# Kernel tuning notes

Measured on AMD Instinct MI355X. Metric: run time of the kernel, lower is better.

The kernel has to match this reference:

```python
import jax, jax.numpy as jnp
import numpy as np

B, S, D, M, HID, THETA = 8, 4096, 128, 256, 256, 4096


def _impulse_response():
    """Build discretized LTI (A,B) via ZOH and the impulse response H [M, S]."""
    Q = jnp.arange(M, dtype=jnp.float32).reshape(-1, 1)          # [M,1]
    R = (2.0 * Q + 1.0) / THETA                                   # [M,1]
    ii, jj = jnp.meshgrid(jnp.arange(M), jnp.arange(M), indexing='ij')
    # (-1)^(i-j+1): -1 when (i-j) even, +1 when odd
    sign = jnp.where((ii - jj) % 2 == 0, -1.0, 1.0)
    A = R * jnp.where(ii < jj, -1.0, sign)                        # [M,M]
    Bv = R * jnp.where(jnp.arange(M).reshape(-1, 1) % 2 == 0, 1.0, -1.0)  # [M,1]
    # zero-order-hold discretization via matrix exponential of augmented system
    aug = jnp.zeros((M + 1, M + 1), dtype=jnp.float32)
    aug = aug.at[:M, :M].set(A).at[:M, M].set(Bv[:, 0])
    expA = jax.scipy.linalg.expm(aug)
    Ad, Bd = expA[:M, :M], expA[:M, M:M + 1]
    # H[:, i] = Ad^i @ Bd
    def step(Ai, _):
        return Ad @ Ai, (Ai @ Bd)[:, 0]
    _, Hs = jax.lax.scan(step, jnp.eye(M, dtype=jnp.float32), None, length=S)
    return Hs.T  # [M, S]


def setup_inputs() -> dict:
    key = jax.random.key(0)
    k1, k2, k3 = jax.random.split(key, 3)
    x = jax.random.normal(k1, (B, S, D), dtype=jnp.float32)
    W_u = jax.random.normal(k2, (D, 1), dtype=jnp.float32) / np.sqrt(D)
    b_u = jnp.zeros((1,), dtype=jnp.float32)
    W_h = jax.random.normal(k3, (M + D, HID), dtype=jnp.float32) / np.sqrt(M + D)
    b_h = jnp.zeros((HID,), dtype=jnp.float32)
    H = _impulse_response()  # [M, S], fixed (non-trainable) impulse response
    return {"x": x, "W_u": W_u, "b_u": b_u, "W_h": W_h, "b_h": b_h, "H": H}


def reference(x, W_u, b_u, W_h, b_h, H):
    batch, seq_len, _ = x.shape
    n = 2 * seq_len
    # u_t = relu(W_u x_t)  -> [B, S, 1]
    u = jax.nn.relu(jnp.einsum('bsd,do->bso', x, W_u) + b_u)
    fft_H = jnp.fft.rfft(H, n=n, axis=-1)                 # [M, S+1]
    fft_u = jnp.fft.rfft(u[..., 0], n=n, axis=-1)         # [B, S+1]
    temp = fft_u[:, None, :] * fft_H[None, :, :]          # [B, M, S+1] complex
    m = jnp.fft.irfft(temp, n=n, axis=-1)[:, :, :seq_len]  # [B, M, S]
    m = jnp.transpose(m, (0, 2, 1))                       # [B, S, M]
    input_h = jnp.concatenate([m, x], axis=-1)            # [B, S, M+D]
    h = jax.nn.relu(jnp.einsum('bsf,fh->bsh', input_h, W_h) + b_h)
    h_n = h[:, -1, :]
    return (h, h_n)
```

## Files before the change

kernel.cpp:

```cpp
#include <hip/hip_runtime.h>

#define S_LEN 4096
#define B_SZ 8
#define HN_OFF 8388608
#define CPROWS 544

typedef __attribute__((ext_vector_type(8))) short short8;
typedef __attribute__((ext_vector_type(4))) float f32x4;

typedef const __attribute__((address_space(1))) unsigned int as1_u32;
typedef __attribute__((address_space(3))) unsigned int as3_u32;

__device__ __forceinline__ void gload16(const short* g, short* l) {
  __builtin_amdgcn_global_load_lds((as1_u32*)g, (as3_u32*)l, 16, 0, 0);
}

__device__ __forceinline__ short f2bf(float f) {
  union { float f; unsigned u; } v; v.f = f;
  unsigned r = v.u + 0x7FFFu + ((v.u >> 16) & 1u);
  return (short)(r >> 16);
}

__global__ __launch_bounds__(256) void k_prep(const float* __restrict__ x,
                                              const float* __restrict__ Wu,
                                              const float* __restrict__ bu,
                                              const float* __restrict__ H,
                                              const float* __restrict__ Wh,
                                              short* __restrict__ cp,
                                              short* __restrict__ xb,
                                              short* __restrict__ Ht,
                                              short* __restrict__ wht) {
  int bx = blockIdx.x;
  if (bx >= 8520) {
    int j = (bx - 8520) * 256 + threadIdx.x;
    if (j < 256 * 384) {
      int n = j / 384, k = j % 384;
      wht[j] = f2bf(Wh[k * 256 + n]);
    }
    return;
  }
  if (bx >= 8264) {
    __shared__ short tile[64][72];
    int bx2 = bx - 8264;
    int t0 = (bx2 >> 2) << 6, q0 = (bx2 & 3) << 6;
    int tid = threadIdx.x;
    int r = tid >> 2, c0 = (tid & 3) << 4;
    const float* src = H + (size_t)(q0 + r) * S_LEN + t0 + c0;
    #pragma unroll
    for (int v4 = 0; v4 < 4; ++v4) {
      float4 hv = *(const float4*)(src + 4 * v4);
      tile[r][c0 + 4 * v4]     = f2bf(hv.x);
      tile[r][c0 + 4 * v4 + 1] = f2bf(hv.y);
      tile[r][c0 + 4 * v4 + 2] = f2bf(hv.z);
      tile[r][c0 + 4 * v4 + 3] = f2bf(hv.w);
    }
    __syncthreads();
    int s2 = tid >> 2, qc = (tid & 3) << 4;
    short8 o0, o1;
    #pragma unroll
    for (int j2 = 0; j2 < 8; ++j2) {
      o0[j2] = tile[qc + j2][s2];
      o1[j2] = tile[qc + 8 + j2][s2];
    }
    short* dst = Ht + (size_t)(t0 + s2) * 256 + q0 + qc;
    *(short8*)dst       = o0;
    *(short8*)(dst + 8) = o1;
    return;
  }
  if (bx >= 8192) {
    int idx = (bx - 8192) * 256 + threadIdx.x;
    if (idx < 18432) {
      int j = idx & 7;
      int r = 508 + ((idx >> 3) % 36);
      int rem = (idx >> 3) / 36;
      int p = rem & 7;
      int b = rem >> 3;
      int e = 8 * r + p + j;
      if (e >= S_LEN)
        cp[((size_t)(b * 8 + p) * CPROWS + r) * 8 + j] = 0;
    }
    return;
  }
  int row = bx * 4 + (threadIdx.x >> 6);
  int l = threadIdx.x & 63;
  float2 xv = *(const float2*)(x + (size_t)row * 128 + 2 * l);
  float2 wv = *(const float2*)(Wu + 2 * l);
  float s = xv.x * wv.x + xv.y * wv.y;
  #pragma unroll
  for (int m = 32; m >= 1; m >>= 1) s += __shfl_xor(s, m, 64);
  unsigned pack = (((unsigned)f2bf(xv.y) & 0xFFFFu) << 16) | ((unsigned)f2bf(xv.x) & 0xFFFFu);
  *(unsigned*)(xb + (size_t)row * 128 + 2 * l) = pack;
  float v = s + bu[0];
  v = v > 0.0f ? v : 0.0f;
  short vb = f2bf(v);
  if (l < 8) {
    int t = row & (S_LEN - 1);
    int b = row >> 12;
    int e = (S_LEN - 1) - t;
    int p = l;
    if (e >= p) {
      int d = e - p;
      cp[((size_t)(b * 8 + p) * CPROWS + (d >> 3)) * 8 + (d & 7)] = vb;
    }
  }
}

__global__ __launch_bounds__(256) void k_g(const short* __restrict__ wht,
                                           const short* __restrict__ Ht,
                                           short* __restrict__ Gt) {
  int nt = blockIdx.x & 1, tt = blockIdx.x >> 1;
  int n0 = nt << 7, t0 = tt << 7;
  int tid = threadIdx.x;
  int lane = tid & 63, wid = tid >> 6;
  int wr = wid >> 1, wc = wid & 1;
  int lm = lane & 15, kg = lane >> 4;

  const short* Abase = wht + (size_t)(n0 + wr * 64 + lm) * 384 + 8 * kg;
  const short* Bbase = Ht  + (size_t)(t0 + wc * 64 + lm) * 256 + 8 * kg;

  f32x4 acc[4][4];
  #pragma unroll
  for (int ii = 0; ii < 4; ++ii)
    #pragma unroll
    for (int jn = 0; jn < 4; ++jn)
      acc[ii][jn] = (f32x4){0.0f, 0.0f, 0.0f, 0.0f};

  #pragma unroll
  for (int c = 0; c < 4; ++c) {
    short8 a[8], bf[8];
    #pragma unroll
    for (int mf = 0; mf < 4; ++mf)
      #pragma unroll
      for (int ks = 0; ks < 2; ++ks)
        a[mf * 2 + ks] = *(const short8*)(Abase + mf * 16 * 384 + c * 64 + ks * 32);
    #pragma unroll
    for (int nf = 0; nf < 4; ++nf)
      #pragma unroll
      for (int ks = 0; ks < 2; ++ks)
        bf[nf * 2 + ks] = *(const short8*)(Bbase + nf * 16 * 256 + c * 64 + ks * 32);
    #pragma unroll
    for (int ks = 0; ks < 2; ++ks)
      #pragma unroll
      for (int mf = 0; mf < 4; ++mf)
        #pragma unroll
        for (int nf = 0; nf < 4; ++nf)
          acc[mf][nf] = __builtin_amdgcn_mfma_f32_16x16x32_bf16(a[mf * 2 + ks], bf[nf * 2 + ks], acc[mf][nf], 0, 0, 0);
  }

  #pragma unroll
  for (int mf = 0; mf < 4; ++mf)
    #pragma unroll
    for (int nf = 0; nf < 4; ++nf)
      #pragma unroll
      for (int j = 0; j < 4; ++j) {
        int n = n0 + wr * 64 + mf * 16 + kg * 4 + j;
        int t = t0 + wc * 64 + nf * 16 + lm;
        Gt[(size_t)n * S_LEN + t] = f2bf(acc[mf][nf][j]);
      }
}

__global__ __launch_bounds__(256, 2) void k_fused(const short* __restrict__ cp,
                                                  const short* __restrict__ Gt,
                                                  const short* __restrict__ xb,
                                                  const short* __restrict__ wht,
                                                  const float* __restrict__ bh,
                                                  float* __restrict__ out) {
  __shared__ __attribute__((aligned(16))) short Bt[2][128 * 128];
  __shared__ __attribute__((aligned(16))) short Aw[2][2048];

  int i = blockIdx.x;
  int j  = i >> 1, lo = i & 1;
  int jj = j & 127;
  int fj = (j >> 7) ? (31 - (jj >> 3)) : (jj >> 3);
  int st = lo ? (31 - fj) : fj;
  int nt = lo;
  int b  = j & 7;
  int s0 = st << 7, n0 = nt << 7;

  int tid = threadIdx.x;
  int lane = tid & 63, wid = tid >> 6;
  int wr = wid >> 1, wc = wid & 1;
  int lm = lane & 15, kg = lane >> 4;
  int l3 = lane >> 3, l7 = lane & 7;
  int lm7 = lm & 7;

  const short* bS0 = Gt + (size_t)(n0 + wid * 32 + kg) * S_LEN + ((lm ^ kg) << 3);
  const short* bS1 = Gt + (size_t)(n0 + wid * 32 + kg) * S_LEN + ((lm ^ kg ^ 4) << 3);

  int asbase = 496 - 16 * st;
  const short* aSrc = cp + ((size_t)(b * 8 + (l7 ^ l3)) * CPROWS + asbase + wid * 8 + l3) * 8;

  const short* xS0 = xb + (size_t)(b * S_LEN + s0 + wid * 32 + kg) * 128 + ((lm ^ kg) << 3);
  const short* xS1 = xb + (size_t)(b * S_LEN + s0 + wid * 32 + kg) * 128 + ((lm ^ kg ^ 4) << 3);

  int dbase = 127 - 64 * wr - lm + 8 * kg;
  int aof[10];
  #pragma unroll
  for (int v = 0; v < 10; ++v) {
    int d = dbase + 16 * v - 48;
    aof[v] = ((d & ~7) | ((d & 7) ^ ((d >> 3) & 7))) << 3;
  }

  int bof[16];
  #pragma unroll
  for (int nf = 0; nf < 4; ++nf)
    #pragma unroll
    for (int ks = 0; ks < 4; ++ks)
      bof[nf * 4 + ks] = (wc * 64 + nf * 16 + lm) * 128 + (((4 * ks + kg) ^ lm7) << 3);

  int aofx[16];
  #pragma unroll
  for (int mf = 0; mf < 4; ++mf)
    #pragma unroll
    for (int ks = 0; ks < 4; ++ks)
      aofx[mf * 4 + ks] = (wr * 64 + mf * 16 + lm) * 128 + (((4 * ks + kg) ^ lm7) << 3);

  f32x4 acc[4][4];
  #pragma unroll
  for (int ii = 0; ii < 4; ++ii)
    #pragma unroll
    for (int jn = 0; jn < 4; ++jn)
      acc[ii][jn] = (f32x4){0.0f, 0.0f, 0.0f, 0.0f};

  int nchunks = st + 1;

  auto STAGE = [&](int cc) {
    int slot = cc & 1;
    int coff = cc * 128;
    #pragma unroll
    for (int e = 0; e < 4; ++e) {
      gload16(bS0 + (size_t)(8 * e) * S_LEN + coff,     &Bt[slot][(wid * 32 + 8 * e) * 128]);
      gload16(bS1 + (size_t)(8 * e + 4) * S_LEN + coff, &Bt[slot][(wid * 32 + 8 * e + 4) * 128]);
    }
    gload16(aSrc + coff, &Aw[slot][wid * 512]);
  };
  auto STAGE_X = [&]() {
    int slot = (st + 1) & 1;
    #pragma unroll
    for (int e = 0; e < 4; ++e) {
      gload16(xS0 + (size_t)(8 * e) * 128,     &Bt[slot][(wid * 32 + 8 * e) * 128]);
      gload16(xS1 + (size_t)(8 * e + 4) * 128, &Bt[slot][(wid * 32 + 8 * e + 4) * 128]);
    }
  };

  STAGE(0);

  for (int c = 0; c < nchunks; ++c) {
    asm volatile("s_waitcnt vmcnt(0) lgkmcnt(0)\n\ts_barrier" ::: "memory");
    if (c + 1 < nchunks) STAGE(c + 1);
    else STAGE_X();
    const short* AwB = &Aw[c & 1][0];
    const short* BtB = &Bt[c & 1][0];
    short8 A10[10];
    #pragma unroll
    for (int v = 0; v < 10; ++v) A10[v] = *(const short8*)(AwB + aof[v]);
    short8 Bf[16];
    #pragma unroll
    for (int ii = 0; ii < 16; ++ii) Bf[ii] = *(const short8*)(BtB + bof[ii]);
    __builtin_amdgcn_s_setprio(1);
    #pragma unroll
    for (int ks = 0; ks < 4; ++ks)
      #pragma unroll
      for (int mf = 0; mf < 4; ++mf)
        #pragma unroll
        for (int nf = 0; nf < 4; ++nf)
          acc[mf][nf] = __builtin_amdgcn_mfma_f32_16x16x32_bf16(
              A10[2 * ks - mf + 3], Bf[nf * 4 + ks], acc[mf][nf], 0, 0, 0);
    __builtin_amdgcn_s_setprio(0);
  }

  short8 Bx[16];
  #pragma unroll
  for (int nf = 0; nf < 4; ++nf)
    #pragma unroll
    for (int ks = 0; ks < 4; ++ks)
      Bx[nf * 4 + ks] = *(const short8*)(wht + (size_t)(n0 + wc * 64 + nf * 16 + lm) * 384 + 256 + 32 * ks + 8 * kg);
  asm volatile("s_waitcnt vmcnt(0) lgkmcnt(0)\n\ts_barrier" ::: "memory");
  {
    const short* XtB = &Bt[(st + 1) & 1][0];
    short8 Ax[16];
    #pragma unroll
    for (int ii = 0; ii < 16; ++ii) Ax[ii] = *(const short8*)(XtB + aofx[ii]);
    __builtin_amdgcn_s_setprio(1);
    #pragma unroll
    for (int ks = 0; ks < 4; ++ks)
      #pragma unroll
      for (int mf = 0; mf < 4; ++mf)
        #pragma unroll
        for (int nf = 0; nf < 4; ++nf)
          acc[mf][nf] = __builtin_amdgcn_mfma_f32_16x16x32_bf16(
              Ax[mf * 4 + ks], Bx[nf * 4 + ks], acc[mf][nf], 0, 0, 0);
    __builtin_amdgcn_s_setprio(0);
  }

  #pragma unroll
  for (int mf = 0; mf < 4; ++mf)
    #pragma unroll
    for (int nf = 0; nf < 4; ++nf) {
      int n = n0 + wc * 64 + nf * 16 + lm;
      float bias = bh[n];
      #pragma unroll
      for (int j2 = 0; j2 < 4; ++j2) {
        int s = s0 + wr * 64 + mf * 16 + kg * 4 + j2;
        float v = acc[mf][nf][j2] + bias;
        v = v > 0.0f ? v : 0.0f;
        out[(size_t)(b * S_LEN + s) * 256 + n] = v;
        if (s == S_LEN - 1)
          out[HN_OFF + b * 256 + n] = v;
      }
    }
}

extern "C" void kernel_launch(void* const* d_in, const int* in_sizes, int n_in,
                              void* d_out, int out_size, void* d_ws, size_t ws_size,
                              hipStream_t stream) {
  const float* x  = (const float*)d_in[0];
  const float* Wu = (const float*)d_in[1];
  const float* bu = (const float*)d_in[2];
  const float* Wh = (const float*)d_in[3];
  const float* bh = (const float*)d_in[4];
  const float* H  = (const float*)d_in[5];
  float* out = (float*)d_out;

  char* ws = (char*)d_ws;
  short* cp  = (short*)(ws);
  short* wht = (short*)(ws + 557056);
  short* xb  = (short*)(ws + 753664);
  short* Ht  = (short*)(ws + 9142272);
  short* Gt  = (short*)(ws + 11239424);

  k_prep<<<8904, 256, 0, stream>>>(x, Wu, bu, H, Wh, cp, xb, Ht, wht);
  k_g   <<<64,   256, 0, stream>>>(wht, Ht, Gt);
  k_fused<<<512, 256, 0, stream>>>(cp, Gt, xb, wht, bh, out);
}
```

Measured before the change: 77.72 us.

## Restructure fused GEMM into 4-slot 64-wide K pipeline with split-phase staging

Changes the fused Toeplitz+x GEMM main loop from a 2-slot buffer of 128-wide K chunks to a 4-slot ring of 64-wide chunks, prefetching two chunks ahead. Waits use partial vmcnt counts instead of draining everything. Each chunk is split into two half-phases that interleave LDS fragment reads, the next stage's global-to-LDS loads and MFMA bursts, separated by barriers. The x·W_h tail is folded into the same loop and its weights are loaded per chunk rather than up front. This aims to overlap memory latency with MFMA work and cut register pressure, at the cost of more barriers and more complex vmcnt bookkeeping.

```diff
diff --git a/kernel.cpp b/kernel.cpp
--- a/kernel.cpp
+++ b/kernel.cpp
@@ -20,6 +20,24 @@
   unsigned r = v.u + 0x7FFFu + ((v.u >> 16) & 1u);
   return (short)(r >> 16);
 }
+
+#define MFMA16(Aa, Bb) \
+  acc[0][0] = __builtin_amdgcn_mfma_f32_16x16x32_bf16(Aa##0, Bb##0, acc[0][0], 0, 0, 0); \
+  acc[0][1] = __builtin_amdgcn_mfma_f32_16x16x32_bf16(Aa##0, Bb##1, acc[0][1], 0, 0, 0); \
+  acc[0][2] = __builtin_amdgcn_mfma_f32_16x16x32_bf16(Aa##0, Bb##2, acc[0][2], 0, 0, 0); \
+  acc[0][3] = __builtin_amdgcn_mfma_f32_16x16x32_bf16(Aa##0, Bb##3, acc[0][3], 0, 0, 0); \
+  acc[1][0] = __builtin_amdgcn_mfma_f32_16x16x32_bf16(Aa##1, Bb##0, acc[1][0], 0, 0, 0); \
+  acc[1][1] = __builtin_amdgcn_mfma_f32_16x16x32_bf16(Aa##1, Bb##1, acc[1][1], 0, 0, 0); \
+  acc[1][2] = __builtin_amdgcn_mfma_f32_16x16x32_bf16(Aa##1, Bb##2, acc[1][2], 0, 0, 0); \
+  acc[1][3] = __builtin_amdgcn_mfma_f32_16x16x32_bf16(Aa##1, Bb##3, acc[1][3], 0, 0, 0); \
+  acc[2][0] = __builtin_amdgcn_mfma_f32_16x16x32_bf16(Aa##2, Bb##0, acc[2][0], 0, 0, 0); \
+  acc[2][1] = __builtin_amdgcn_mfma_f32_16x16x32_bf16(Aa##2, Bb##1, acc[2][1], 0, 0, 0); \
+  acc[2][2] = __builtin_amdgcn_mfma_f32_16x16x32_bf16(Aa##2, Bb##2, acc[2][2], 0, 0, 0); \
+  acc[2][3] = __builtin_amdgcn_mfma_f32_16x16x32_bf16(Aa##2, Bb##3, acc[2][3], 0, 0, 0); \
+  acc[3][0] = __builtin_amdgcn_mfma_f32_16x16x32_bf16(Aa##3, Bb##0, acc[3][0], 0, 0, 0); \
+  acc[3][1] = __builtin_amdgcn_mfma_f32_16x16x32_bf16(Aa##3, Bb##1, acc[3][1], 0, 0, 0); \
+  acc[3][2] = __builtin_amdgcn_mfma_f32_16x16x32_bf16(Aa##3, Bb##2, acc[3][2], 0, 0, 0); \
+  acc[3][3] = __builtin_amdgcn_mfma_f32_16x16x32_bf16(Aa##3, Bb##3, acc[3][3], 0, 0, 0);
 
 __global__ __launch_bounds__(256) void k_prep(const float* __restrict__ x,
                                               const float* __restrict__ Wu,
@@ -165,8 +183,8 @@
                                                   const short* __restrict__ wht,
                                                   const float* __restrict__ bh,
                                                   float* __restrict__ out) {
-  __shared__ __attribute__((aligned(16))) short Bt[2][128 * 128];
-  __shared__ __attribute__((aligned(16))) short Aw[2][2048];
+  __shared__ __attribute__((aligned(16))) short Bt[4][128 * 64];
+  __shared__ __attribute__((aligned(16))) short Aw[4][2048];
 
   int i = blockIdx.x;
   int j  = i >> 1, lo = i & 1;
@@ -184,36 +202,32 @@
   int l3 = lane >> 3, l7 = lane & 7;
   int lm7 = lm & 7;
 
-  const short* bS0 = Gt + (size_t)(n0 + wid * 32 + kg) * S_LEN + ((lm ^ kg) << 3);
-  const short* bS1 = Gt + (size_t)(n0 + wid * 32 + kg) * S_LEN + ((lm ^ kg ^ 4) << 3);
-
+  const short* bSrc = Gt + (size_t)(n0 + wid * 32 + l3) * S_LEN + ((l7 ^ l3) << 3);
   int asbase = 496 - 16 * st;
   const short* aSrc = cp + ((size_t)(b * 8 + (l7 ^ l3)) * CPROWS + asbase + wid * 8 + l3) * 8;
-
-  const short* xS0 = xb + (size_t)(b * S_LEN + s0 + wid * 32 + kg) * 128 + ((lm ^ kg) << 3);
-  const short* xS1 = xb + (size_t)(b * S_LEN + s0 + wid * 32 + kg) * 128 + ((lm ^ kg ^ 4) << 3);
+  const short* xSrc = xb + (size_t)(b * S_LEN + s0 + wid * 32 + l3) * 128 + ((l7 ^ l3) << 3);
 
   int dbase = 127 - 64 * wr - lm + 8 * kg;
-  int aof[10];
-  #pragma unroll
-  for (int v = 0; v < 10; ++v) {
-    int d = dbase + 16 * v - 48;
-    aof[v] = ((d & ~7) | ((d & 7) ^ ((d >> 3) & 7))) << 3;
-  }
-
-  int bof[16];
+  int aof[6];
+  #pragma unroll
+  for (int ii = 0; ii < 6; ++ii) {
+    int d = (ii < 4) ? (dbase - 16 * ii) : (dbase + 96 - 16 * ii);
+    aof[ii] = ((d & ~7) | ((d & 7) ^ ((d >> 3) & 7))) << 3;
+  }
+  int bRow = (wc * 64 + lm) * 64;
+  int bof[8];
   #pragma unroll
   for (int nf = 0; nf < 4; ++nf)
     #pragma unroll
-    for (int ks = 0; ks < 4; ++ks)
-      bof[nf * 4 + ks] = (wc * 64 + nf * 16 + lm) * 128 + (((4 * ks + kg) ^ lm7) << 3);
-
-  int aofx[16];
+    for (int ks = 0; ks < 2; ++ks)
+      bof[nf * 2 + ks] = bRow + nf * 1024 + (((ks << 5) + (kg << 3)) ^ (lm7 << 3));
+  int xof[8];
   #pragma unroll
   for (int mf = 0; mf < 4; ++mf)
     #pragma unroll
-    for (int ks = 0; ks < 4; ++ks)
-      aofx[mf * 4 + ks] = (wr * 64 + mf * 16 + lm) * 128 + (((4 * ks + kg) ^ lm7) << 3);
+    for (int ks = 0; ks < 2; ++ks)
+      xof[mf * 2 + ks] = (wr * 64 + mf * 16 + lm) * 64 + (((ks << 5) + (kg << 3)) ^ (lm7 << 3));
+  const short* wxBase = wht + (size_t)(n0 + wc * 64 + lm) * 384 + 256 + 8 * kg;
 
   f32x4 acc[4][4];
   #pragma unroll
@@ -222,75 +236,101 @@
     for (int jn = 0; jn < 4; ++jn)
       acc[ii][jn] = (f32x4){0.0f, 0.0f, 0.0f, 0.0f};
 
-  int nchunks = st + 1;
-
-  auto STAGE = [&](int cc) {
-    int slot = cc & 1;
-    int coff = cc * 128;
-    #pragma unroll
-    for (int e = 0; e < 4; ++e) {
-      gload16(bS0 + (size_t)(8 * e) * S_LEN + coff,     &Bt[slot][(wid * 32 + 8 * e) * 128]);
-      gload16(bS1 + (size_t)(8 * e + 4) * S_LEN + coff, &Bt[slot][(wid * 32 + 8 * e + 4) * 128]);
-    }
-    gload16(aSrc + coff, &Aw[slot][wid * 512]);
+  int T  = 2 * st + 2;
+  int NC = T + 2;
+
+  auto STAGE_T = [&](int cc, int part) {
+    int slot = cc & 3;
+    if (part == 0) {
+      gload16(bSrc + cc * 64,                         &Bt[slot][(wid * 32) * 64]);
+      gload16(bSrc + (size_t)8 * S_LEN + cc * 64,     &Bt[slot][(wid * 32 + 8) * 64]);
+      gload16(aSrc + cc * 64,                         &Aw[slot][wid * 512]);
+    } else {
+      gload16(bSrc + (size_t)16 * S_LEN + cc * 64,    &Bt[slot][(wid * 32 + 16) * 64]);
+      gload16(bSrc + (size_t)24 * S_LEN + cc * 64,    &Bt[slot][(wid * 32 + 24) * 64]);
+    }
   };
-  auto STAGE_X = [&]() {
-    int slot = (st + 1) & 1;
-    #pragma unroll
-    for (int e = 0; e < 4; ++e) {
-      gload16(xS0 + (size_t)(8 * e) * 128,     &Bt[slot][(wid * 32 + 8 * e) * 128]);
-      gload16(xS1 + (size_t)(8 * e + 4) * 128, &Bt[slot][(wid * 32 + 8 * e + 4) * 128]);
+  auto STAGE_X = [&](int cc, int part) {
+    int slot = cc & 3;
+    int co = (cc - T) * 64;
+    if (part == 0) {
+      gload16(xSrc + co,              &Bt[slot][(wid * 32) * 64]);
+      gload16(xSrc + co + 8 * 128,    &Bt[slot][(wid * 32 + 8) * 64]);
+    } else {
+      gload16(xSrc + co + 16 * 128,   &Bt[slot][(wid * 32 + 16) * 64]);
+      gload16(xSrc + co + 24 * 128,   &Bt[slot][(wid * 32 + 24) * 64]);
     }
   };
 
-  STAGE(0);
-
-  for (int c = 0; c < nchunks; ++c) {
-    asm volatile("s_waitcnt vmcnt(0) lgkmcnt(0)\n\ts_barrier" ::: "memory");
-    if (c + 1 < nchunks) STAGE(c + 1);
-    else STAGE_X();
-    const short* AwB = &Aw[c & 1][0];
-    const short* BtB = &Bt[c & 1][0];
-    short8 A10[10];
-    #pragma unroll
-    for (int v = 0; v < 10; ++v) A10[v] = *(const short8*)(AwB + aof[v]);
-    short8 Bf[16];
-    #pragma unroll
-    for (int ii = 0; ii < 16; ++ii) Bf[ii] = *(const short8*)(BtB + bof[ii]);
-    __builtin_amdgcn_s_setprio(1);
-    #pragma unroll
-    for (int ks = 0; ks < 4; ++ks)
-      #pragma unroll
-      for (int mf = 0; mf < 4; ++mf)
-        #pragma unroll
-        for (int nf = 0; nf < 4; ++nf)
-          acc[mf][nf] = __builtin_amdgcn_mfma_f32_16x16x32_bf16(
-              A10[2 * ks - mf + 3], Bf[nf * 4 + ks], acc[mf][nf], 0, 0, 0);
-    __builtin_amdgcn_s_setprio(0);
-  }
-
-  short8 Bx[16];
-  #pragma unroll
-  for (int nf = 0; nf < 4; ++nf)
-    #pragma unroll
-    for (int ks = 0; ks < 4; ++ks)
-      Bx[nf * 4 + ks] = *(const short8*)(wht + (size_t)(n0 + wc * 64 + nf * 16 + lm) * 384 + 256 + 32 * ks + 8 * kg);
-  asm volatile("s_waitcnt vmcnt(0) lgkmcnt(0)\n\ts_barrier" ::: "memory");
-  {
-    const short* XtB = &Bt[(st + 1) & 1][0];
-    short8 Ax[16];
-    #pragma unroll
-    for (int ii = 0; ii < 16; ++ii) Ax[ii] = *(const short8*)(XtB + aofx[ii]);
-    __builtin_amdgcn_s_setprio(1);
-    #pragma unroll
-    for (int ks = 0; ks < 4; ++ks)
-      #pragma unroll
-      for (int mf = 0; mf < 4; ++mf)
-        #pragma unroll
-        for (int nf = 0; nf < 4; ++nf)
-          acc[mf][nf] = __builtin_amdgcn_mfma_f32_16x16x32_bf16(
-              Ax[mf * 4 + ks], Bx[nf * 4 + ks], acc[mf][nf], 0, 0, 0);
-    __builtin_amdgcn_s_setprio(0);
+  STAGE_T(0, 0); STAGE_T(0, 1);
+  STAGE_T(1, 0); STAGE_T(1, 1);
+
+  for (int c = 0; c < NC; ++c) {
+    if (c + 1 < T)       asm volatile("s_waitcnt vmcnt(5)\n\ts_barrier" ::: "memory");
+    else if (c + 1 < NC) asm volatile("s_waitcnt vmcnt(4)\n\ts_barrier" ::: "memory");
+    else                 asm volatile("s_waitcnt vmcnt(0)\n\ts_barrier" ::: "memory");
+
+    const short* BtB = &Bt[c & 3][0];
+    if (c < T) {
+      const short* AwB = &Aw[c & 3][0];
+      short8 A0 = *(const short8*)(AwB + aof[0]);
+      short8 A1 = *(const short8*)(AwB + aof[1]);
+      short8 A2 = *(const short8*)(AwB + aof[2]);
+      short8 A3 = *(const short8*)(AwB + aof[3]);
+      short8 B0 = *(const short8*)(BtB + bof[0]);
+      short8 B1 = *(const short8*)(BtB + bof[2]);
+      short8 B2 = *(const short8*)(BtB + bof[4]);
+      short8 B3 = *(const short8*)(BtB + bof[6]);
+      if (c + 2 < T) STAGE_T(c + 2, 0);
+      else if (c + 2 < NC) STAGE_X(c + 2, 0);
+      asm volatile("s_barrier" ::: "memory");
+      __builtin_amdgcn_s_setprio(1);
+      MFMA16(A, B)
+      __builtin_amdgcn_s_setprio(0);
+      asm volatile("s_barrier" ::: "memory");
+      short8 C0 = *(const short8*)(AwB + aof[4]);
+      short8 C1 = *(const short8*)(AwB + aof[5]);
+      short8 C2 = A0, C3 = A1;
+      short8 D0 = *(const short8*)(BtB + bof[1]);
+      short8 D1 = *(const short8*)(BtB + bof[3]);
+      short8 D2 = *(const short8*)(BtB + bof[5]);
+      short8 D3 = *(const short8*)(BtB + bof[7]);
+      if (c + 2 < T) STAGE_T(c + 2, 1);
+      else if (c + 2 < NC) STAGE_X(c + 2, 1);
+      asm volatile("s_barrier" ::: "memory");
+      __builtin_amdgcn_s_setprio(1);
+      MFMA16(C, D)
+      __builtin_amdgcn_s_setprio(0);
+      asm volatile("s_barrier" ::: "memory");
+    } else {
+      int co = (c - T) * 64;
+      short8 A0 = *(const short8*)(BtB + xof[0]);
+      short8 A1 = *(const short8*)(BtB + xof[2]);
+      short8 A2 = *(const short8*)(BtB + xof[4]);
+      short8 A3 = *(const short8*)(BtB + xof[6]);
+      short8 B0 = *(const short8*)(wxBase + co);
+      short8 B1 = *(const short8*)(wxBase + 16 * 384 + co);
+      short8 B2 = *(const short8*)(wxBase + 32 * 384 + co);
+      short8 B3 = *(const short8*)(wxBase + 48 * 384 + co);
+      asm volatile("s_barrier" ::: "memory");
+      __builtin_amdgcn_s_setprio(1);
+      MFMA16(A, B)
+      __builtin_amdgcn_s_setprio(0);
+      asm volatile("s_barrier" ::: "memory");
+      short8 C0 = *(const short8*)(BtB + xof[1]);
+      short8 C1 = *(const short8*)(BtB + xof[3]);
+      short8 C2 = *(const short8*)(BtB + xof[5]);
+      short8 C3 = *(const short8*)(BtB + xof[7]);
+      short8 D0 = *(const short8*)(wxBase + co + 32);
+      short8 D1 = *(const short8*)(wxBase + 16 * 384 + co + 32);
+      short8 D2 = *(const short8*)(wxBase + 32 * 384 + co + 32);
+      short8 D3 = *(const short8*)(wxBase + 48 * 384 + co + 32);
+      asm volatile("s_barrier" ::: "memory");
+      __builtin_amdgcn_s_setprio(1);
+      MFMA16(C, D)
+      __builtin_amdgcn_s_setprio(0);
+      asm volatile("s_barrier" ::: "memory");
+    }
   }
 
   #pragma unroll
```

Measured after the change: 82.42 us. 6.1% more time.

## Pair triangular tiles per 512-thread block in fused kernel

Applied to the files above, without the earlier changes.

The fused Toeplitz-GEMM kernel now launches 256 blocks of 512 threads (8 waves) instead of 512 blocks of 256. Each block handles two complementary sequence tiles (st and 31-st) one after another, so every block does the same total amount of triangular work. Wave tiles shrink to 64x32, the x-projection GEMM is folded into the same chunk loop as a final iteration, and the Aw buffer is enlarged. This aims to balance load and raise wave occupancy per block, but it serializes the two phases and adds extra barriers.

```diff
diff --git a/kernel.cpp b/kernel.cpp
--- a/kernel.cpp
+++ b/kernel.cpp
@@ -159,39 +159,30 @@
       }
 }
 
-__global__ __launch_bounds__(256, 2) void k_fused(const short* __restrict__ cp,
+__global__ __launch_bounds__(512, 2) void k_fused(const short* __restrict__ cp,
                                                   const short* __restrict__ Gt,
                                                   const short* __restrict__ xb,
                                                   const short* __restrict__ wht,
                                                   const float* __restrict__ bh,
                                                   float* __restrict__ out) {
   __shared__ __attribute__((aligned(16))) short Bt[2][128 * 128];
-  __shared__ __attribute__((aligned(16))) short Aw[2][2048];
+  __shared__ __attribute__((aligned(16))) short Aw[2][6144];
 
   int i = blockIdx.x;
-  int j  = i >> 1, lo = i & 1;
-  int jj = j & 127;
-  int fj = (j >> 7) ? (31 - (jj >> 3)) : (jj >> 3);
-  int st = lo ? (31 - fj) : fj;
-  int nt = lo;
-  int b  = j & 7;
-  int s0 = st << 7, n0 = nt << 7;
+  int kk = i >> 4;
+  int nt = i & 1;
+  int b  = (i >> 1) & 7;
+  int n0 = nt << 7;
 
   int tid = threadIdx.x;
   int lane = tid & 63, wid = tid >> 6;
-  int wr = wid >> 1, wc = wid & 1;
+  int wr = wid >> 2, wc = wid & 3;
   int lm = lane & 15, kg = lane >> 4;
   int l3 = lane >> 3, l7 = lane & 7;
   int lm7 = lm & 7;
 
-  const short* bS0 = Gt + (size_t)(n0 + wid * 32 + kg) * S_LEN + ((lm ^ kg) << 3);
-  const short* bS1 = Gt + (size_t)(n0 + wid * 32 + kg) * S_LEN + ((lm ^ kg ^ 4) << 3);
-
-  int asbase = 496 - 16 * st;
-  const short* aSrc = cp + ((size_t)(b * 8 + (l7 ^ l3)) * CPROWS + asbase + wid * 8 + l3) * 8;
-
-  const short* xS0 = xb + (size_t)(b * S_LEN + s0 + wid * 32 + kg) * 128 + ((lm ^ kg) << 3);
-  const short* xS1 = xb + (size_t)(b * S_LEN + s0 + wid * 32 + kg) * 128 + ((lm ^ kg ^ 4) << 3);
+  const short* bS0 = Gt + (size_t)(n0 + wid * 16 + kg) * S_LEN + ((lm ^ kg) << 3);
+  const short* bS1 = Gt + (size_t)(n0 + wid * 16 + 4 + kg) * S_LEN + ((lm ^ (kg ^ 4)) << 3);
 
   int dbase = 127 - 64 * wr - lm + 8 * kg;
   int aof[10];
@@ -201,114 +192,127 @@
     aof[v] = ((d & ~7) | ((d & 7) ^ ((d >> 3) & 7))) << 3;
   }
 
-  int bof[16];
-  #pragma unroll
-  for (int nf = 0; nf < 4; ++nf)
+  int bof[8];
+  #pragma unroll
+  for (int nf = 0; nf < 2; ++nf)
     #pragma unroll
     for (int ks = 0; ks < 4; ++ks)
-      bof[nf * 4 + ks] = (wc * 64 + nf * 16 + lm) * 128 + (((4 * ks + kg) ^ lm7) << 3);
-
-  int aofx[16];
+      bof[nf * 4 + ks] = (wc * 32 + nf * 16 + lm) * 128 + (((4 * ks + kg) ^ lm7) << 3);
+
+  int xof[16];
   #pragma unroll
   for (int mf = 0; mf < 4; ++mf)
     #pragma unroll
     for (int ks = 0; ks < 4; ++ks)
-      aofx[mf * 4 + ks] = (wr * 64 + mf * 16 + lm) * 128 + (((4 * ks + kg) ^ lm7) << 3);
-
-  f32x4 acc[4][4];
-  #pragma unroll
-  for (int ii = 0; ii < 4; ++ii)
-    #pragma unroll
-    for (int jn = 0; jn < 4; ++jn)
-      acc[ii][jn] = (f32x4){0.0f, 0.0f, 0.0f, 0.0f};
-
-  int nchunks = st + 1;
-
-  auto STAGE = [&](int cc) {
-    int slot = cc & 1;
-    int coff = cc * 128;
-    #pragma unroll
-    for (int e = 0; e < 4; ++e) {
-      gload16(bS0 + (size_t)(8 * e) * S_LEN + coff,     &Bt[slot][(wid * 32 + 8 * e) * 128]);
-      gload16(bS1 + (size_t)(8 * e + 4) * S_LEN + coff, &Bt[slot][(wid * 32 + 8 * e + 4) * 128]);
-    }
-    gload16(aSrc + coff, &Aw[slot][wid * 512]);
-  };
-  auto STAGE_X = [&]() {
-    int slot = (st + 1) & 1;
-    #pragma unroll
-    for (int e = 0; e < 4; ++e) {
-      gload16(xS0 + (size_t)(8 * e) * 128,     &Bt[slot][(wid * 32 + 8 * e) * 128]);
-      gload16(xS1 + (size_t)(8 * e + 4) * 128, &Bt[slot][(wid * 32 + 8 * e + 4) * 128]);
-    }
-  };
-
-  STAGE(0);
-
-  for (int c = 0; c < nchunks; ++c) {
+      xof[mf * 4 + ks] = (wr * 64 + mf * 16 + lm) * 128 + (((4 * ks + kg) ^ lm7) << 3);
+
+  const short* wxBase = wht + (size_t)(n0 + wc * 32 + lm) * 384 + 256 + 8 * kg;
+
+  for (int ph = 0; ph < 2; ++ph) {
+    int st = ph ? kk : (31 - kk);
+    int s0 = st << 7;
+    int asbase = 496 - 16 * st;
+    const short* aSrc = cp + ((size_t)(b * 8 + (l7 ^ l3)) * CPROWS + asbase + wid * 8 + l3) * 8;
+    const short* xR0 = xb + (size_t)(b * S_LEN + s0 + wid * 16 + kg) * 128 + ((lm ^ kg) << 3);
+    const short* xR1 = xb + (size_t)(b * S_LEN + s0 + wid * 16 + 4 + kg) * 128 + ((lm ^ (kg ^ 4)) << 3);
+
+    int NCt = st + 1;
+    int NCp = NCt + 1;
+
+    f32x4 acc[4][2];
+    #pragma unroll
+    for (int ii = 0; ii < 4; ++ii)
+      #pragma unroll
+      for (int jn = 0; jn < 2; ++jn)
+        acc[ii][jn] = (f32x4){0.0f, 0.0f, 0.0f, 0.0f};
+
+    auto STAGE_T = [&](int cc) {
+      int slot = cc & 1;
+      int coff = cc * 128;
+      #pragma unroll
+      for (int e = 0; e < 2; ++e) {
+        gload16(bS0 + (size_t)(8 * e) * S_LEN + coff, &Bt[slot][(wid * 16 + 8 * e) * 128]);
+        gload16(bS1 + (size_t)(8 * e) * S_LEN + coff, &Bt[slot][(wid * 16 + 8 * e + 4) * 128]);
+      }
+      if (wid < 4) gload16(aSrc + coff, &Aw[slot][wid * 512]);
+    };
+    auto STAGE_X = [&]() {
+      int slot = NCt & 1;
+      #pragma unroll
+      for (int e = 0; e < 2; ++e) {
+        gload16(xR0 + (size_t)(8 * e) * 128, &Bt[slot][(wid * 16 + 8 * e) * 128]);
+        gload16(xR1 + (size_t)(8 * e) * 128, &Bt[slot][(wid * 16 + 8 * e + 4) * 128]);
+      }
+    };
+
     asm volatile("s_waitcnt vmcnt(0) lgkmcnt(0)\n\ts_barrier" ::: "memory");
-    if (c + 1 < nchunks) STAGE(c + 1);
-    else STAGE_X();
-    const short* AwB = &Aw[c & 1][0];
-    const short* BtB = &Bt[c & 1][0];
-    short8 A10[10];
-    #pragma unroll
-    for (int v = 0; v < 10; ++v) A10[v] = *(const short8*)(AwB + aof[v]);
-    short8 Bf[16];
-    #pragma unroll
-    for (int ii = 0; ii < 16; ++ii) Bf[ii] = *(const short8*)(BtB + bof[ii]);
-    __builtin_amdgcn_s_setprio(1);
-    #pragma unroll
-    for (int ks = 0; ks < 4; ++ks)
-      #pragma unroll
-      for (int mf = 0; mf < 4; ++mf)
-        #pragma unroll
-        for (int nf = 0; nf < 4; ++nf)
-          acc[mf][nf] = __builtin_amdgcn_mfma_f32_16x16x32_bf16(
-              A10[2 * ks - mf + 3], Bf[nf * 4 + ks], acc[mf][nf], 0, 0, 0);
-    __builtin_amdgcn_s_setprio(0);
-  }
-
-  short8 Bx[16];
-  #pragma unroll
-  for (int nf = 0; nf < 4; ++nf)
-    #pragma unroll
-    for (int ks = 0; ks < 4; ++ks)
-      Bx[nf * 4 + ks] = *(const short8*)(wht + (size_t)(n0 + wc * 64 + nf * 16 + lm) * 384 + 256 + 32 * ks + 8 * kg);
-  asm volatile("s_waitcnt vmcnt(0) lgkmcnt(0)\n\ts_barrier" ::: "memory");
-  {
-    const short* XtB = &Bt[(st + 1) & 1][0];
-    short8 Ax[16];
-    #pragma unroll
-    for (int ii = 0; ii < 16; ++ii) Ax[ii] = *(const short8*)(XtB + aofx[ii]);
-    __builtin_amdgcn_s_setprio(1);
-    #pragma unroll
-    for (int ks = 0; ks < 4; ++ks)
-      #pragma unroll
-      for (int mf = 0; mf < 4; ++mf)
-        #pragma unroll
-        for (int nf = 0; nf < 4; ++nf)
-          acc[mf][nf] = __builtin_amdgcn_mfma_f32_16x16x32_bf16(
-              Ax[mf * 4 + ks], Bx[nf * 4 + ks], acc[mf][nf], 0, 0, 0);
-    __builtin_amdgcn_s_setprio(0);
-  }
-
-  #pragma unroll
-  for (int mf = 0; mf < 4; ++mf)
-    #pragma unroll
-    for (int nf = 0; nf < 4; ++nf) {
-      int n = n0 + wc * 64 + nf * 16 + lm;
-      float bias = bh[n];
-      #pragma unroll
-      for (int j2 = 0; j2 < 4; ++j2) {
-        int s = s0 + wr * 64 + mf * 16 + kg * 4 + j2;
-        float v = acc[mf][nf][j2] + bias;
-        v = v > 0.0f ? v : 0.0f;
-        out[(size_t)(b * S_LEN + s) * 256 + n] = v;
-        if (s == S_LEN - 1)
-          out[HN_OFF + b * 256 + n] = v;
-      }
-    }
+    STAGE_T(0);
+
+    for (int c = 0; c < NCp; ++c) {
+      asm volatile("s_waitcnt vmcnt(0) lgkmcnt(0)\n\ts_barrier" ::: "memory");
+      if (c + 1 < NCt) STAGE_T(c + 1);
+      else if (c + 1 < NCp) STAGE_X();
+
+      if (c < NCt) {
+        const short* AwB = &Aw[c & 1][0];
+        const short* BtB = &Bt[c & 1][0];
+        short8 A10[10];
+        #pragma unroll
+        for (int v = 0; v < 10; ++v) A10[v] = *(const short8*)(AwB + aof[v]);
+        short8 Bf[8];
+        #pragma unroll
+        for (int ii = 0; ii < 8; ++ii) Bf[ii] = *(const short8*)(BtB + bof[ii]);
+        __builtin_amdgcn_s_setprio(1);
+        #pragma unroll
+        for (int ks = 0; ks < 4; ++ks)
+          #pragma unroll
+          for (int mf = 0; mf < 4; ++mf)
+            #pragma unroll
+            for (int nf = 0; nf < 2; ++nf)
+              acc[mf][nf] = __builtin_amdgcn_mfma_f32_16x16x32_bf16(
+                  A10[2 * ks - mf + 3], Bf[nf * 4 + ks], acc[mf][nf], 0, 0, 0);
+        __builtin_amdgcn_s_setprio(0);
+      } else {
+        const short* BtB = &Bt[NCt & 1][0];
+        short8 Ax[16];
+        #pragma unroll
+        for (int ii = 0; ii < 16; ++ii) Ax[ii] = *(const short8*)(BtB + xof[ii]);
+        short8 Bx[8];
+        #pragma unroll
+        for (int nf = 0; nf < 2; ++nf)
+          #pragma unroll
+          for (int ks = 0; ks < 4; ++ks)
+            Bx[nf * 4 + ks] = *(const short8*)(wxBase + (size_t)nf * 16 * 384 + 32 * ks);
+        __builtin_amdgcn_s_setprio(1);
+        #pragma unroll
+        for (int ks = 0; ks < 4; ++ks)
+          #pragma unroll
+          for (int mf = 0; mf < 4; ++mf)
+            #pragma unroll
+            for (int nf = 0; nf < 2; ++nf)
+              acc[mf][nf] = __builtin_amdgcn_mfma_f32_16x16x32_bf16(
+                  Ax[mf * 4 + ks], Bx[nf * 4 + ks], acc[mf][nf], 0, 0, 0);
+        __builtin_amdgcn_s_setprio(0);
+      }
+    }
+
+    #pragma unroll
+    for (int mf = 0; mf < 4; ++mf)
+      #pragma unroll
+      for (int nf = 0; nf < 2; ++nf) {
+        int n = n0 + wc * 32 + nf * 16 + lm;
+        float bias = bh[n];
+        #pragma unroll
+        for (int j2 = 0; j2 < 4; ++j2) {
+          int s = s0 + wr * 64 + mf * 16 + kg * 4 + j2;
+          float v = acc[mf][nf][j2] + bias;
+          v = v > 0.0f ? v : 0.0f;
+          out[(size_t)(b * S_LEN + s) * 256 + n] = v;
+          if (s == S_LEN - 1)
+            out[HN_OFF + b * 256 + n] = v;
+        }
+      }
+  }
 }
 
 extern "C" void kernel_launch(void* const* d_in, const int* in_sizes, int n_in,
@@ -331,5 +335,5 @@
 
   k_prep<<<8904, 256, 0, stream>>>(x, Wu, bu, H, Wh, cp, xb, Ht, wht);
   k_g   <<<64,   256, 0, stream>>>(wht, Ht, Gt);
-  k_fused<<<512, 256, 0, stream>>>(cp, Gt, xb, wht, bh, out);
-}
+  k_fused<<<256, 512, 0, stream>>>(cp, Gt, xb, wht, bh, out);
+}
```

New measurement: 76.34 us. Within noise of the previous version (-1.8%).
